# Kernel optimization log

Hardware: AMD Instinct MI355X
Metric: run time of the kernel (lower is better)

The kernel has to match this reference:

```python
import jax, jax.numpy as jnp
import numpy as np

B, S, D, H = 2, 2048, 1024, 16
DH = D // H


def setup_inputs() -> dict:
    key = jax.random.key(0)
    ks = jax.random.split(key, 9)
    s = 0.02
    return {
        "x": jax.random.normal(ks[0], (B, S, D), dtype=jnp.float32),
        "Wq": jax.random.normal(ks[1], (D, D), dtype=jnp.float32) * s,
        "bq": jnp.zeros((D,), dtype=jnp.float32),
        "Wk": jax.random.normal(ks[2], (D, D), dtype=jnp.float32) * s,
        "bk": jnp.zeros((D,), dtype=jnp.float32),
        "Wv": jax.random.normal(ks[3], (D, D), dtype=jnp.float32) * s,
        "bv": jnp.zeros((D,), dtype=jnp.float32),
        "Wo": jax.random.normal(ks[4], (D, D), dtype=jnp.float32) * s,
        "bo": jnp.zeros((D,), dtype=jnp.float32),
    }


def _split_heads(t):
    # [B,S,D] -> [B,H,S,Dh]
    return t.reshape(B, S, H, DH).transpose(0, 2, 1, 3)


def reference(x, Wq, bq, Wk, bk, Wv, bv, Wo, bo):
    q = _split_heads(x @ Wq + bq)
    k = _split_heads(x @ Wk + bk)
    v = _split_heads(x @ Wv + bv)
    scale = 1.0 / jnp.sqrt(jnp.float32(DH))
    # [B,H,S,S] attention scores (naive, materialized as in original)
    scores = jnp.einsum("bhqd,bhkd->bhqk", q, k) * scale
    probs = jax.nn.softmax(scores, axis=-1)
    attn = jnp.einsum("bhqk,bhkd->bhqd", probs, v)
    out = attn.transpose(0, 2, 1, 3).reshape(B, S, D)
    return out @ Wo + bo
```

## Files before the change

### kernel.cpp

```cpp
#include <hip/hip_runtime.h>
#include <math.h>

#define NB 2
#define NS 2048
#define ND 1024
#define NH 16
#define NDH 64
#define NM (NB * NS)
#define K2 (2 * ND)

typedef unsigned short ushortT;
typedef __attribute__((ext_vector_type(8))) short bf16x8;
typedef __attribute__((ext_vector_type(4))) float f32x4;
typedef __attribute__((ext_vector_type(16))) float f32x16;

__device__ inline unsigned short f2bf(float f) {
    union { float f; unsigned u; } v; v.f = f;
    unsigned r = v.u + 0x7FFFu + ((v.u >> 16) & 1u);
    return (unsigned short)(r >> 16);
}
__device__ inline float bf2f(unsigned short h) {
    union { unsigned u; float f; } v; v.u = ((unsigned)h) << 16; return v.f;
}
__device__ inline void gl_lds16(const ushortT* g, ushortT* l) {
    __builtin_amdgcn_global_load_lds(
        (const __attribute__((address_space(1))) unsigned*)g,
        (__attribute__((address_space(3))) unsigned*)l, 16, 0, 0);
}

__global__ __launch_bounds__(256) void split_x(
    const float* __restrict__ x, ushortT* __restrict__ xh)
{
    int idx = (blockIdx.x * 256 + threadIdx.x) * 4;
    float4 v = *(const float4*)&x[idx];
    float fv[4] = {v.x, v.y, v.z, v.w};
    union { ushortT s[4]; uint2 u; } o;
#pragma unroll
    for (int j = 0; j < 4; ++j) o.s[j] = f2bf(fv[j]);
    *(uint2*)&xh[idx] = o.u;
}

__global__ __launch_bounds__(256) void split_w_t(
    const float* __restrict__ Wq, const float* __restrict__ Wk,
    const float* __restrict__ Wv, const float* __restrict__ Wo,
    ushortT* __restrict__ WtH, ushortT* __restrict__ WtO)
{
    const int z = blockIdx.z;
    const float* __restrict__ W = (z == 0) ? Wq : (z == 1) ? Wk : (z == 2) ? Wv : Wo;

    const int k0 = blockIdx.y * 64, n0 = blockIdx.x * 64;
    const int t = threadIdx.x;
    __shared__ float Ls[64][65];

#pragma unroll
    for (int i = 0; i < 4; ++i) {
        int kl = i * 16 + (t >> 4);
        int nl = (t & 15) << 2;
        float4 w4 = *(const float4*)&W[(size_t)(k0 + kl) * ND + n0 + nl];
        Ls[nl + 0][kl] = w4.x;
        Ls[nl + 1][kl] = w4.y;
        Ls[nl + 2][kl] = w4.z;
        Ls[nl + 3][kl] = w4.w;
    }
    __syncthreads();
#pragma unroll
    for (int i = 0; i < 16; ++i) {
        int flat = i * 256 + t;
        int n = flat >> 6, kk = flat & 63;
        float val = Ls[n][kk];
        unsigned short hi = f2bf(val);
        if (z < 3) {
            WtH[(size_t)z * ND * ND + (size_t)(n0 + n) * ND + (k0 + kk)] = hi;
        } else {
            WtO[(size_t)(n0 + n) * K2 + (k0 + kk)]      = hi;
            WtO[(size_t)(n0 + n) * K2 + ND + (k0 + kk)] = f2bf(val - bf2f(hi));
        }
    }
}

template <int OUTMODE>
__global__ __launch_bounds__(256) void gemm_split(
    const ushortT* __restrict__ A2,
    const ushortT* __restrict__ Wt,
    const float* __restrict__ b0, const float* __restrict__ b1, const float* __restrict__ b2,
    ushortT* __restrict__ Qo, ushortT* __restrict__ Ko, ushortT* __restrict__ Vtg,
    float* __restrict__ Ofp)
{
    const int z = blockIdx.z;
    const int AS = OUTMODE ? K2 : ND;
    const ushortT* __restrict__ Bt = OUTMODE ? Wt : Wt + (size_t)z * ND * ND;
    const float* __restrict__ bias = (z == 0) ? b0 : (z == 1) ? b1 : b2;

    const int m0 = blockIdx.y * 128;
    const int n0 = blockIdx.x * 128;
    const int tid = threadIdx.x;
    const int lane = tid & 63, w = tid >> 6;
    const int wrow = w >> 1, wcol = w & 1;
    const int a = lane & 15, g = lane >> 4;

    __shared__ __align__(16) ushortT Abuf[128 * 32];
    __shared__ __align__(16) ushortT Bbuf[128 * 32];

    f32x4 acc[4][4] = {};

    const int srow_l = tid >> 2;
    const int scc0 = tid & 3;
    const int swz = (a >> 1) & 3;

    const int NSTEP = OUTMODE ? 96 : 32;
    for (int ks = 0; ks < NSTEP; ++ks) {
        const int kp = ks * 32;
        const int ac = OUTMODE ? ((kp < ND) ? kp : kp - ND) : kp;
        const int bc = OUTMODE ? ((kp < 2 * ND) ? kp : kp - 2 * ND) : kp;
        __syncthreads();
#pragma unroll
        for (int t = 0; t < 2; ++t) {
            int r = t * 64 + srow_l;
            int sc = scc0 ^ ((r >> 1) & 3);
            gl_lds16(&A2[(size_t)(m0 + r) * AS + ac + (sc << 3)],
                     &Abuf[(t * 256 + w * 64) * 8]);
            gl_lds16(&Bt[(size_t)(n0 + r) * AS + bc + (sc << 3)],
                     &Bbuf[(t * 256 + w * 64) * 8]);
        }
        __syncthreads();

        bf16x8 af[4], bfr[4];
#pragma unroll
        for (int i = 0; i < 4; ++i)
            af[i] = *(const bf16x8*)&Abuf[(wrow * 64 + i * 16 + a) * 32 + ((g ^ swz) << 3)];
#pragma unroll
        for (int j = 0; j < 4; ++j)
            bfr[j] = *(const bf16x8*)&Bbuf[(wcol * 64 + j * 16 + a) * 32 + ((g ^ swz) << 3)];
#pragma unroll
        for (int i = 0; i < 4; ++i)
#pragma unroll
            for (int j = 0; j < 4; ++j)
                acc[i][j] = __builtin_amdgcn_mfma_f32_16x16x32_bf16(af[i], bfr[j], acc[i][j], 0, 0, 0);
    }

    float bj[4];
#pragma unroll
    for (int j = 0; j < 4; ++j) bj[j] = bias[n0 + wcol * 64 + j * 16 + a];

#pragma unroll
    for (int i = 0; i < 4; ++i) {
#pragma unroll
        for (int r = 0; r < 4; ++r) {
            int grow = m0 + wrow * 64 + i * 16 + g * 4 + r;
#pragma unroll
            for (int j = 0; j < 4; ++j) {
                int gcol = n0 + wcol * 64 + j * 16 + a;
                float v = acc[i][j][r] + bj[j];
                if (OUTMODE == 1) {
                    Ofp[(size_t)grow * ND + gcol] = v;
                } else {
                    int b = grow >> 11, s = grow & (NS - 1);
                    int h = gcol >> 6, dh = gcol & 63;
                    if (z < 2) {
                        ushortT* dst = (z == 0) ? Qo : Ko;
                        dst[((size_t)(b * NH + h) * NS + s) * NDH + dh] = f2bf(v);
                    } else {
                        Vtg[((size_t)(b * NH + h) * NDH + dh) * NS + s] = f2bf(v);
                    }
                }
            }
        }
    }
}

__global__ __launch_bounds__(256) void attn_fwd2(
    const ushortT* __restrict__ Q, const ushortT* __restrict__ K,
    const ushortT* __restrict__ Vt, ushortT* __restrict__ A2o)
{
    const int bh = blockIdx.y;
    const int b = bh >> 4, h = bh & 15;
    const int q0 = blockIdx.x * 128;
    const int tid = threadIdx.x, lane = tid & 63, w = tid >> 6;
    const int ql = lane & 31;
    const int hi = lane >> 5;

    __shared__ __align__(16) unsigned smem4[8192];
    ushortT* sK = (ushortT*)smem4;
    ushortT* sV = sK + 2 * 4096;

    const ushortT* __restrict__ Kb  = K  + (size_t)bh * NS * NDH;
    const ushortT* __restrict__ Vtb = Vt + (size_t)bh * NDH * NS;

    bf16x8 qf[4];
    {
        const ushortT* qrow = Q + (size_t)bh * NS * NDH + (size_t)(q0 + w * 32 + ql) * NDH + hi * 8;
#pragma unroll
        for (int kc = 0; kc < 4; ++kc) {
            qf[kc] = *(const bf16x8*)(qrow + kc * 16);
#pragma unroll
            for (int j = 0; j < 8; ++j)
                qf[kc][j] = (short)f2bf(bf2f((ushortT)qf[kc][j]) * 0.125f);
        }
    }

    const int srw = lane >> 3;
    const int scc = lane & 7;

    float m_run = -INFINITY, l_run = 0.f;
    f32x16 oat[2] = {};

#pragma unroll
    for (int c = 0; c < 2; ++c) {
        int rK = c * 32 + w * 8 + srw;
        gl_lds16(&Kb[(size_t)rK * NDH + ((scc ^ srw) << 3)], &sK[(c * 256 + w * 64) * 8]);
        gl_lds16(&Vtb[(size_t)rK * NS + ((scc ^ srw) << 3)], &sV[(c * 256 + w * 64) * 8]);
    }

    for (int t = 0; t < NS / 64; ++t) {
        const int cur = t & 1;
        __syncthreads();
        if (t + 1 < NS / 64) {
            const int nxt = cur ^ 1;
            const int kv1 = (t + 1) * 64;
#pragma unroll
            for (int c = 0; c < 2; ++c) {
                int rK = c * 32 + w * 8 + srw;
                gl_lds16(&Kb[(size_t)(kv1 + rK) * NDH + ((scc ^ srw) << 3)],
                         &sK[(nxt * 4096) + (c * 256 + w * 64) * 8]);
                gl_lds16(&Vtb[(size_t)rK * NS + kv1 + ((scc ^ srw) << 3)],
                         &sV[(nxt * 4096) + (c * 256 + w * 64) * 8]);
            }
        }
        const ushortT* kbuf = sK + cur * 4096;
        const ushortT* vbuf = sV + cur * 4096;

        f32x16 st[2] = {};
#pragma unroll
        for (int s = 0; s < 2; ++s) {
            const int kv = s * 32 + ql;
#pragma unroll
            for (int kc = 0; kc < 4; ++kc) {
                bf16x8 kf = *(const bf16x8*)&kbuf[kv * 64 + (((kc * 2 + hi) ^ (ql & 7)) << 3)];
                st[s] = __builtin_amdgcn_mfma_f32_32x32x16_bf16(kf, qf[kc], st[s], 0, 0, 0);
            }
        }

        float mx = -INFINITY;
#pragma unroll
        for (int s = 0; s < 2; ++s)
#pragma unroll
            for (int r = 0; r < 16; ++r) mx = fmaxf(mx, st[s][r]);
        mx = fmaxf(mx, __shfl_xor(mx, 32));
        float mn = fmaxf(m_run, mx);
        float al = __expf(m_run - mn);
        float rs = 0.f;
#pragma unroll
        for (int s = 0; s < 2; ++s)
#pragma unroll
            for (int r = 0; r < 16; ++r) {
                float e = __expf(st[s][r] - mn);
                st[s][r] = e;
                rs += e;
            }
        rs += __shfl_xor(rs, 32);
        l_run = l_run * al + rs;
        m_run = mn;
#pragma unroll
        for (int dt = 0; dt < 2; ++dt)
#pragma unroll
            for (int r = 0; r < 16; ++r) oat[dt][r] *= al;

#pragma unroll
        for (int ts = 0; ts < 4; ++ts) {
            const int s = ts >> 1, rb = 8 * (ts & 1);
            unsigned u0 = (unsigned)f2bf(st[s][rb + 0]) | ((unsigned)f2bf(st[s][rb + 1]) << 16);
            unsigned u1 = (unsigned)f2bf(st[s][rb + 2]) | ((unsigned)f2bf(st[s][rb + 3]) << 16);
            unsigned v0 = (unsigned)f2bf(st[s][rb + 4]) | ((unsigned)f2bf(st[s][rb + 5]) << 16);
            unsigned v1 = (unsigned)f2bf(st[s][rb + 6]) | ((unsigned)f2bf(st[s][rb + 7]) << 16);
            unsigned t0 = hi ? u0 : v0;
            unsigned t1 = hi ? u1 : v1;
            unsigned t0s = __shfl_xor(t0, 32);
            unsigned t1s = __shfl_xor(t1, 32);
            union { unsigned u[4]; bf16x8 v; } pf;
            pf.u[0] = hi ? t0s : u0;
            pf.u[1] = hi ? t1s : u1;
            pf.u[2] = hi ? v0 : t0s;
            pf.u[3] = hi ? v1 : t1s;
#pragma unroll
            for (int dt = 0; dt < 2; ++dt) {
                bf16x8 vf = *(const bf16x8*)&vbuf[(dt * 32 + ql) * 64 + (((ts * 2 + hi) ^ (ql & 7)) << 3)];
                oat[dt] = __builtin_amdgcn_mfma_f32_32x32x16_bf16(vf, pf.v, oat[dt], 0, 0, 0);
            }
        }
    }

    __syncthreads();
    unsigned* osc = smem4 + w * 2048;
    float inv = 1.0f / l_run;
#pragma unroll
    for (int dt = 0; dt < 2; ++dt)
#pragma unroll
        for (int r = 0; r < 16; ++r) {
            int d = dt * 32 + (r & 3) + 8 * (r >> 2) + 4 * hi;
            float o = oat[dt][r] * inv;
            unsigned short hb = f2bf(o);
            unsigned short lb = f2bf(o - bf2f(hb));
            osc[ql * 64 + (d ^ ql)] = (unsigned)hb | ((unsigned)lb << 16);
        }
    __syncthreads();
    const int qrd = lane >> 3;
    const int dbase = (lane & 7) * 8;
#pragma unroll
    for (int p = 0; p < 4; ++p) {
        int q = p * 8 + qrd;
        unsigned wv[8];
#pragma unroll
        for (int k = 0; k < 8; ++k)
            wv[k] = osc[q * 64 + ((dbase + k) ^ q)];
        union { ushortT s[8]; bf16x8 v; } hs, ls;
#pragma unroll
        for (int k = 0; k < 8; ++k) {
            hs.s[k] = (ushortT)(wv[k] & 0xffffu);
            ls.s[k] = (ushortT)(wv[k] >> 16);
        }
        size_t row = (size_t)(b * NS + q0 + w * 32 + q) * K2 + h * 64 + dbase;
        *(bf16x8*)&A2o[row]      = hs.v;
        *(bf16x8*)&A2o[row + ND] = ls.v;
    }
}

extern "C" void kernel_launch(void* const* d_in, const int* in_sizes, int n_in,
                              void* d_out, int out_size, void* d_ws, size_t ws_size,
                              hipStream_t stream)
{
    const float* x  = (const float*)d_in[0];
    const float* Wq = (const float*)d_in[1];
    const float* bq = (const float*)d_in[2];
    const float* Wk = (const float*)d_in[3];
    const float* bk = (const float*)d_in[4];
    const float* Wv = (const float*)d_in[5];
    const float* bv = (const float*)d_in[6];
    const float* Wo = (const float*)d_in[7];
    const float* bo = (const float*)d_in[8];
    float* out = (float*)d_out;

    ushortT* xh  = (ushortT*)d_ws;
    ushortT* WtH = xh  + (size_t)NM * ND;
    ushortT* WtO = WtH + (size_t)3 * ND * ND;
    ushortT* Qb  = WtO + (size_t)ND * K2;
    ushortT* Kb  = Qb  + (size_t)NM * ND;
    ushortT* Vtg = Kb  + (size_t)NM * ND;
    ushortT* A2  = Vtg + (size_t)NM * ND;

    split_x<<<dim3(NM * ND / 1024), 256, 0, stream>>>(x, xh);
    split_w_t<<<dim3(16, 16, 4), 256, 0, stream>>>(Wq, Wk, Wv, Wo, WtH, WtO);
    gemm_split<0><<<dim3(8, 32, 3), 256, 0, stream>>>(
        xh, WtH, bq, bk, bv, Qb, Kb, Vtg, nullptr);
    attn_fwd2<<<dim3(NS / 128, NB * NH), 256, 0, stream>>>(Qb, Kb, Vtg, A2);
    gemm_split<1><<<dim3(8, 32, 1), 256, 0, stream>>>(
        A2, WtO, bo, bo, bo, nullptr, nullptr, nullptr, out);
}
```

Measured before the change: 255.7 us.

## Double-buffer GEMM LDS tiles and streamline attention softmax with exp2 and lazy rescale

```diff
diff --git a/kernel.cpp b/kernel.cpp
--- a/kernel.cpp
+++ b/kernel.cpp
@@ -22,11 +22,19 @@
 __device__ inline float bf2f(unsigned short h) {
     union { unsigned u; float f; } v; v.u = ((unsigned)h) << 16; return v.f;
 }
+__device__ inline unsigned cvt_pk_bf16(float lo, float hi) {
+    unsigned r;
+    asm("v_cvt_pk_bf16_f32 %0, %1, %2" : "=v"(r) : "v"(lo), "v"(hi));
+    return r;
+}
 __device__ inline void gl_lds16(const ushortT* g, ushortT* l) {
     __builtin_amdgcn_global_load_lds(
         (const __attribute__((address_space(1))) unsigned*)g,
         (__attribute__((address_space(3))) unsigned*)l, 16, 0, 0);
 }
+#define VM0_BARRIER() asm volatile("s_waitcnt vmcnt(0)\ns_barrier" ::: "memory")
+
+#define QSC 0.18033688011112042f
 
 __global__ __launch_bounds__(256) void split_x(
     const float* __restrict__ x, ushortT* __restrict__ xh)
@@ -98,8 +106,8 @@
     const int wrow = w >> 1, wcol = w & 1;
     const int a = lane & 15, g = lane >> 4;
 
-    __shared__ __align__(16) ushortT Abuf[128 * 32];
-    __shared__ __align__(16) ushortT Bbuf[128 * 32];
+    __shared__ __align__(16) ushortT Abuf[2][128 * 32];
+    __shared__ __align__(16) ushortT Bbuf[2][128 * 32];
 
     f32x4 acc[4][4] = {};
 
@@ -107,35 +115,43 @@
     const int scc0 = tid & 3;
     const int swz = (a >> 1) & 3;
 
-    const int NSTEP = OUTMODE ? 96 : 32;
-    for (int ks = 0; ks < NSTEP; ++ks) {
+    const int nst = OUTMODE ? 96 : 32;
+
+    auto stage = [&](int bufi, int ks) {
         const int kp = ks * 32;
         const int ac = OUTMODE ? ((kp < ND) ? kp : kp - ND) : kp;
         const int bc = OUTMODE ? ((kp < 2 * ND) ? kp : kp - 2 * ND) : kp;
-        __syncthreads();
 #pragma unroll
         for (int t = 0; t < 2; ++t) {
             int r = t * 64 + srow_l;
             int sc = scc0 ^ ((r >> 1) & 3);
             gl_lds16(&A2[(size_t)(m0 + r) * AS + ac + (sc << 3)],
-                     &Abuf[(t * 256 + w * 64) * 8]);
+                     &Abuf[bufi][(t * 256 + w * 64) * 8]);
             gl_lds16(&Bt[(size_t)(n0 + r) * AS + bc + (sc << 3)],
-                     &Bbuf[(t * 256 + w * 64) * 8]);
-        }
-        __syncthreads();
+                     &Bbuf[bufi][(t * 256 + w * 64) * 8]);
+        }
+    };
+
+    stage(0, 0);
+    VM0_BARRIER();
+    for (int i = 0; i < nst; ++i) {
+        const int cur = i & 1;
+        if (i + 1 < nst) stage(cur ^ 1, i + 1);
 
         bf16x8 af[4], bfr[4];
 #pragma unroll
-        for (int i = 0; i < 4; ++i)
-            af[i] = *(const bf16x8*)&Abuf[(wrow * 64 + i * 16 + a) * 32 + ((g ^ swz) << 3)];
+        for (int ii = 0; ii < 4; ++ii)
+            af[ii] = *(const bf16x8*)&Abuf[cur][(wrow * 64 + ii * 16 + a) * 32 + ((g ^ swz) << 3)];
 #pragma unroll
         for (int j = 0; j < 4; ++j)
-            bfr[j] = *(const bf16x8*)&Bbuf[(wcol * 64 + j * 16 + a) * 32 + ((g ^ swz) << 3)];
-#pragma unroll
-        for (int i = 0; i < 4; ++i)
+            bfr[j] = *(const bf16x8*)&Bbuf[cur][(wcol * 64 + j * 16 + a) * 32 + ((g ^ swz) << 3)];
+#pragma unroll
+        for (int ii = 0; ii < 4; ++ii)
 #pragma unroll
             for (int j = 0; j < 4; ++j)
-                acc[i][j] = __builtin_amdgcn_mfma_f32_16x16x32_bf16(af[i], bfr[j], acc[i][j], 0, 0, 0);
+                acc[ii][j] = __builtin_amdgcn_mfma_f32_16x16x32_bf16(af[ii], bfr[j], acc[ii][j], 0, 0, 0);
+
+        VM0_BARRIER();
     }
 
     float bj[4];
@@ -156,9 +172,10 @@
                 } else {
                     int b = grow >> 11, s = grow & (NS - 1);
                     int h = gcol >> 6, dh = gcol & 63;
-                    if (z < 2) {
-                        ushortT* dst = (z == 0) ? Qo : Ko;
-                        dst[((size_t)(b * NH + h) * NS + s) * NDH + dh] = f2bf(v);
+                    if (z == 0) {
+                        Qo[((size_t)(b * NH + h) * NS + s) * NDH + dh] = f2bf(v * QSC);
+                    } else if (z == 1) {
+                        Ko[((size_t)(b * NH + h) * NS + s) * NDH + dh] = f2bf(v);
                     } else {
                         Vtg[((size_t)(b * NH + h) * NDH + dh) * NS + s] = f2bf(v);
                     }
@@ -190,12 +207,7 @@
     {
         const ushortT* qrow = Q + (size_t)bh * NS * NDH + (size_t)(q0 + w * 32 + ql) * NDH + hi * 8;
 #pragma unroll
-        for (int kc = 0; kc < 4; ++kc) {
-            qf[kc] = *(const bf16x8*)(qrow + kc * 16);
-#pragma unroll
-            for (int j = 0; j < 8; ++j)
-                qf[kc][j] = (short)f2bf(bf2f((ushortT)qf[kc][j]) * 0.125f);
-        }
+        for (int kc = 0; kc < 4; ++kc) qf[kc] = *(const bf16x8*)(qrow + kc * 16);
     }
 
     const int srw = lane >> 3;
@@ -246,32 +258,36 @@
 #pragma unroll
             for (int r = 0; r < 16; ++r) mx = fmaxf(mx, st[s][r]);
         mx = fmaxf(mx, __shfl_xor(mx, 32));
-        float mn = fmaxf(m_run, mx);
-        float al = __expf(m_run - mn);
+
+        if (!__all(mx - m_run <= 8.0f)) {
+            float mn = fmaxf(m_run, mx);
+            float al = __builtin_amdgcn_exp2f(m_run - mn);
+            m_run = mn;
+            l_run *= al;
+#pragma unroll
+            for (int dt = 0; dt < 2; ++dt)
+#pragma unroll
+                for (int r = 0; r < 16; ++r) oat[dt][r] *= al;
+        }
         float rs = 0.f;
 #pragma unroll
         for (int s = 0; s < 2; ++s)
 #pragma unroll
             for (int r = 0; r < 16; ++r) {
-                float e = __expf(st[s][r] - mn);
+                float e = __builtin_amdgcn_exp2f(st[s][r] - m_run);
                 st[s][r] = e;
                 rs += e;
             }
         rs += __shfl_xor(rs, 32);
-        l_run = l_run * al + rs;
-        m_run = mn;
-#pragma unroll
-        for (int dt = 0; dt < 2; ++dt)
-#pragma unroll
-            for (int r = 0; r < 16; ++r) oat[dt][r] *= al;
+        l_run += rs;
 
 #pragma unroll
         for (int ts = 0; ts < 4; ++ts) {
             const int s = ts >> 1, rb = 8 * (ts & 1);
-            unsigned u0 = (unsigned)f2bf(st[s][rb + 0]) | ((unsigned)f2bf(st[s][rb + 1]) << 16);
-            unsigned u1 = (unsigned)f2bf(st[s][rb + 2]) | ((unsigned)f2bf(st[s][rb + 3]) << 16);
-            unsigned v0 = (unsigned)f2bf(st[s][rb + 4]) | ((unsigned)f2bf(st[s][rb + 5]) << 16);
-            unsigned v1 = (unsigned)f2bf(st[s][rb + 6]) | ((unsigned)f2bf(st[s][rb + 7]) << 16);
+            unsigned u0 = cvt_pk_bf16(st[s][rb + 0], st[s][rb + 1]);
+            unsigned u1 = cvt_pk_bf16(st[s][rb + 2], st[s][rb + 3]);
+            unsigned v0 = cvt_pk_bf16(st[s][rb + 4], st[s][rb + 5]);
+            unsigned v1 = cvt_pk_bf16(st[s][rb + 6], st[s][rb + 7]);
             unsigned t0 = hi ? u0 : v0;
             unsigned t1 = hi ? u1 : v1;
             unsigned t0s = __shfl_xor(t0, 32);
```

Measured after the change: 272.2 us. +6.5%, slower.
